# Kernel optimization log

Measured on AMD Instinct MI355X. Metric: run time of the kernel, lower is better.

The kernel has to match this reference:

```python
import jax, jax.numpy as jnp
import numpy as np

R, N, F, L = 4, 4096, 64, 2  # relations, entities, feature dim, conv layers


def setup_inputs() -> dict:
    key = jax.random.key(0)
    k_adj, k_feat, k_w, k_rel = jax.random.split(key, 4)
    adjacency = jax.random.uniform(k_adj, (R, N, N), dtype=jnp.float32)
    features = jax.random.normal(k_feat, (N, F), dtype=jnp.float32)
    # per-layer conv weights, torch.rand init: [L, R, F_out, F_in]
    conv_weights = jax.random.uniform(k_w, (L, R, F, F), dtype=jnp.float32)
    # DistMult relation matrices initialized as diag(rand(F)) per torch code
    diag_vals = jax.random.uniform(k_rel, (R, F), dtype=jnp.float32)
    rel_matrices = jax.vmap(jnp.diag)(diag_vals)  # [R, F, F]
    return {
        "adjacency": adjacency,
        "features": features,
        "conv_weights": conv_weights,
        "rel_matrices": rel_matrices,
    }


def reference(adjacency, features, conv_weights, rel_matrices):
    x = features  # [N, F]
    for l in range(conv_weights.shape[0]):
        # sum_r A[r] @ x @ W[l,r].T  -> [N, F]
        agg = jnp.einsum("rnm,mf->rnf", adjacency, x)
        y = jnp.einsum("rnf,rgf->ng", agg, conv_weights[l])
        x = jax.nn.sigmoid(y)
    # DistMult: res[r] = x @ M_r @ x.T  -> [R, N, N]
    xm = jnp.einsum("nf,rfg->rng", x, rel_matrices)
    return jnp.einsum("rng,mg->rnm", xm, x)
```

## Files before the change

### kernel.cpp

```cpp
#include <hip/hip_runtime.h>
#include <hip/hip_bf16.h>

#define NN 4096
#define FF 64
#define RR 4
#define KS 4

typedef __attribute__((ext_vector_type(8))) short bf16x8;
typedef __attribute__((ext_vector_type(4))) float f32x4;

__device__ __forceinline__ short f2bf(float f) {
  unsigned u = __builtin_bit_cast(unsigned, f);
  u = (u + 0x7fffu + ((u >> 16) & 1u)) >> 16;
  return (short)u;
}
__device__ __forceinline__ float bf2f(short s) {
  unsigned u = ((unsigned)(unsigned short)s) << 16;
  return __builtin_bit_cast(float, u);
}

__global__ void rgcn_prep(const float* __restrict__ feat, short* __restrict__ xfrag) {
  int kb = blockIdx.x;
  int t = threadIdx.x >> 6;
  int lane = threadIdx.x & 63;
  int lg = lane >> 4, li = lane & 15;
  bf16x8 pack;
#pragma unroll
  for (int e = 0; e < 8; e++) {
    int row = kb * 32 + lg * 8 + e;
    int col = t * 16 + li;
    pack[e] = f2bf(feat[row * FF + col]);
  }
  *(bf16x8*)(xfrag + (((size_t)(kb * 4 + t) * 64) + lane) * 8) = pack;
}

__global__ __launch_bounds__(256) void rgcn_agg(const float* __restrict__ A,
                                                const short* __restrict__ xfrag,
                                                float* __restrict__ aggp) {
  int w = threadIdx.x >> 6, lane = threadIdx.x & 63;
  int lg = lane >> 4, li = lane & 15;
  int r = blockIdx.y, ks = blockIdx.z;
  int n0 = blockIdx.x * 64 + w * 16;
  const float* Arow = A + ((size_t)r * NN + (n0 + li)) * NN;

  f32x4 acc0 = 0.f, acc1 = 0.f, acc2 = 0.f, acc3 = 0.f;

#pragma unroll 2
  for (int kk = 0; kk < 1024 / 32; kk++) {
    int k0 = ks * 1024 + kk * 32;
    const float4* pa = (const float4*)(Arow + k0 + lg * 8);
    float4 v0 = pa[0], v1 = pa[1];
    bf16x8 a;
    a[0] = f2bf(v0.x); a[1] = f2bf(v0.y); a[2] = f2bf(v0.z); a[3] = f2bf(v0.w);
    a[4] = f2bf(v1.x); a[5] = f2bf(v1.y); a[6] = f2bf(v1.z); a[7] = f2bf(v1.w);
    int kb = k0 >> 5;
    const short* xb = xfrag + (size_t)kb * 4 * 64 * 8 + lane * 8;
    bf16x8 b0 = *(const bf16x8*)(xb + 0 * 64 * 8);
    bf16x8 b1 = *(const bf16x8*)(xb + 1 * 64 * 8);
    bf16x8 b2 = *(const bf16x8*)(xb + 2 * 64 * 8);
    bf16x8 b3 = *(const bf16x8*)(xb + 3 * 64 * 8);
    acc0 = __builtin_amdgcn_mfma_f32_16x16x32_bf16(a, b0, acc0, 0, 0, 0);
    acc1 = __builtin_amdgcn_mfma_f32_16x16x32_bf16(a, b1, acc1, 0, 0, 0);
    acc2 = __builtin_amdgcn_mfma_f32_16x16x32_bf16(a, b2, acc2, 0, 0, 0);
    acc3 = __builtin_amdgcn_mfma_f32_16x16x32_bf16(a, b3, acc3, 0, 0, 0);
  }

  int pidx = ks * RR + r;
  float* out = aggp + ((size_t)pidx * NN + n0) * FF;
  f32x4 accs[4] = {acc0, acc1, acc2, acc3};
#pragma unroll
  for (int t = 0; t < 4; t++)
#pragma unroll
    for (int i = 0; i < 4; i++)
      out[(4 * lg + i) * FF + t * 16 + li] = accs[t][i];
}

__global__ __launch_bounds__(256) void rgcn_combine(const float* __restrict__ aggp,
                                                    const float* __restrict__ W,
                                                    short* __restrict__ xbf,
                                                    short* __restrict__ xfrag) {
  __shared__ float Wt[RR * FF * FF];
  int tid = threadIdx.x;
  for (int idx = tid; idx < RR * FF * FF; idx += 256) {
    int r = idx >> 12, g = (idx >> 6) & 63, f = idx & 63;
    Wt[(r * FF + f) * FF + g] = W[idx];
  }
  __syncthreads();

  int nl = tid >> 6, g = tid & 63;
  int n = blockIdx.x * 4 + nl;
  float acc = 0.f;
  for (int ksr = 0; ksr < KS * RR; ksr++) {
    int r = ksr & 3;
    float av = aggp[((size_t)ksr * NN + n) * FF + g];
#pragma unroll
    for (int f = 0; f < FF; f++)
      acc += __shfl(av, f) * Wt[(r * FF + f) * FF + g];
  }
  float xv = 1.f / (1.f + __expf(-acc));
  xbf[n * FF + g] = f2bf(xv);
  int kb = n >> 5, kr = n & 31, lg2 = kr >> 3, e = kr & 7, t = g >> 4, li = g & 15;
  xfrag[(((size_t)(kb * 4 + t) * 64) + lg2 * 16 + li) * 8 + e] = f2bf(xv);
}

__global__ __launch_bounds__(256) void rgcn_xm(const short* __restrict__ xbf,
                                               const float* __restrict__ M,
                                               short* __restrict__ xm) {
  __shared__ float Ml[FF * FF];
  int tid = threadIdx.x;
  int r = blockIdx.y;
  for (int idx = tid; idx < FF * FF; idx += 256) Ml[idx] = M[r * FF * FF + idx];
  __syncthreads();
  int nl = tid >> 6, g = tid & 63;
  int n = blockIdx.x * 4 + nl;
  float xv = bf2f(xbf[n * FF + g]);
  float acc = 0.f;
#pragma unroll
  for (int f = 0; f < FF; f++) acc += __shfl(xv, f) * Ml[f * FF + g];
  xm[((size_t)r * NN + n) * FF + g] = f2bf(acc);
}

__global__ __launch_bounds__(256) void rgcn_distmult(const short* __restrict__ xm,
                                                     const short* __restrict__ xbf,
                                                     float* __restrict__ out) {
  int w = threadIdx.x >> 6, lane = threadIdx.x & 63;
  int lg = lane >> 4, li = lane & 15;
  int r = blockIdx.z;
  int n0 = blockIdx.y * 64 + w * 16;
  int m0 = blockIdx.x * 64;

  const short* pa = xm + ((size_t)r * NN + n0 + li) * FF + lg * 8;
  bf16x8 a0 = *(const bf16x8*)(pa);
  bf16x8 a1 = *(const bf16x8*)(pa + 32);

  f32x4 acc0 = 0.f, acc1 = 0.f, acc2 = 0.f, acc3 = 0.f;
#pragma unroll
  for (int s = 0; s < 2; s++) {
    bf16x8 af = (s == 0) ? a0 : a1;
    const short* pb = xbf + (size_t)(m0 + li) * FF + s * 32 + lg * 8;
    bf16x8 b0 = *(const bf16x8*)(pb + 0 * 16 * FF);
    bf16x8 b1 = *(const bf16x8*)(pb + 1 * 16 * FF);
    bf16x8 b2 = *(const bf16x8*)(pb + 2 * 16 * FF);
    bf16x8 b3 = *(const bf16x8*)(pb + 3 * 16 * FF);
    acc0 = __builtin_amdgcn_mfma_f32_16x16x32_bf16(af, b0, acc0, 0, 0, 0);
    acc1 = __builtin_amdgcn_mfma_f32_16x16x32_bf16(af, b1, acc1, 0, 0, 0);
    acc2 = __builtin_amdgcn_mfma_f32_16x16x32_bf16(af, b2, acc2, 0, 0, 0);
    acc3 = __builtin_amdgcn_mfma_f32_16x16x32_bf16(af, b3, acc3, 0, 0, 0);
  }
  f32x4 accs[4] = {acc0, acc1, acc2, acc3};
#pragma unroll
  for (int t = 0; t < 4; t++)
#pragma unroll
    for (int i = 0; i < 4; i++)
      out[((size_t)r * NN + (n0 + 4 * lg + i)) * NN + m0 + t * 16 + li] = accs[t][i];
}

extern "C" void kernel_launch(void* const* d_in, const int* in_sizes, int n_in,
                              void* d_out, int out_size, void* d_ws, size_t ws_size,
                              hipStream_t stream) {
  const float* A = (const float*)d_in[0];
  const float* feat = (const float*)d_in[1];
  const float* Wc = (const float*)d_in[2];
  const float* M = (const float*)d_in[3];
  float* out = (float*)d_out;

  char* ws = (char*)d_ws;
  short* xfrag = (short*)ws;
  short* xbf   = (short*)(ws + (512 << 10));
  short* xmb   = (short*)(ws + (1 << 20));
  float* aggp = (float*)d_out;

  rgcn_prep<<<dim3(128), 256, 0, stream>>>(feat, xfrag);
  for (int l = 0; l < 2; l++) {
    rgcn_agg<<<dim3(64, RR, KS), 256, 0, stream>>>(A, xfrag, aggp);
    rgcn_combine<<<dim3(NN / 4), 256, 0, stream>>>(aggp, Wc + (size_t)l * RR * FF * FF, xbf, xfrag);
  }
  rgcn_xm<<<dim3(NN / 4, RR), 256, 0, stream>>>(xbf, M, xmb);
  rgcn_distmult<<<dim3(64, 64, RR), 256, 0, stream>>>(xmb, xbf, out);
}
```

Baseline: 784.3 us.

## Reassociate RGCN layer as A@(xW^T) with atomic accumulation across relations

```diff
diff --git a/kernel.cpp b/kernel.cpp
--- a/kernel.cpp
+++ b/kernel.cpp
@@ -19,29 +19,39 @@
   return __builtin_bit_cast(float, u);
 }
 
-__global__ void rgcn_prep(const float* __restrict__ feat, short* __restrict__ xfrag) {
-  int kb = blockIdx.x;
-  int t = threadIdx.x >> 6;
-  int lane = threadIdx.x & 63;
-  int lg = lane >> 4, li = lane & 15;
-  bf16x8 pack;
+__global__ __launch_bounds__(256) void rgcn_z(const float* __restrict__ x,
+                                              const float* __restrict__ W,
+                                              short* __restrict__ zfrag,
+                                              float* __restrict__ y) {
+  int tid = threadIdx.x;
+  int r = blockIdx.y;
+  int gtid = (blockIdx.y * (NN / 4) + blockIdx.x) * 256 + tid;
+  if (gtid < NN * FF) y[gtid] = 0.f;
+
+  int nl = tid >> 6, g = tid & 63;
+  int n = blockIdx.x * 4 + nl;
+  const float* xr = x + n * FF;
+  const float* wr = W + (r * FF + g) * FF;
+  float acc = 0.f;
 #pragma unroll
-  for (int e = 0; e < 8; e++) {
-    int row = kb * 32 + lg * 8 + e;
-    int col = t * 16 + li;
-    pack[e] = f2bf(feat[row * FF + col]);
+  for (int f = 0; f < FF; f += 4) {
+    float4 xv = *(const float4*)(xr + f);
+    float4 wv = *(const float4*)(wr + f);
+    acc += xv.x * wv.x + xv.y * wv.y + xv.z * wv.z + xv.w * wv.w;
   }
-  *(bf16x8*)(xfrag + (((size_t)(kb * 4 + t) * 64) + lane) * 8) = pack;
+  int kb = n >> 5, r5 = n & 31, lg = r5 >> 3, e = r5 & 7, t = g >> 4, li = g & 15;
+  zfrag[(size_t)r * NN * FF + (((kb * 4 + t) * 64) + lg * 16 + li) * 8 + e] = f2bf(acc);
 }
 
 __global__ __launch_bounds__(256) void rgcn_agg(const float* __restrict__ A,
-                                                const short* __restrict__ xfrag,
-                                                float* __restrict__ aggp) {
+                                                const short* __restrict__ zfrag,
+                                                float* __restrict__ y) {
   int w = threadIdx.x >> 6, lane = threadIdx.x & 63;
   int lg = lane >> 4, li = lane & 15;
   int r = blockIdx.y, ks = blockIdx.z;
   int n0 = blockIdx.x * 64 + w * 16;
   const float* Arow = A + ((size_t)r * NN + (n0 + li)) * NN;
+  const short* zf = zfrag + (size_t)r * NN * FF;
 
   f32x4 acc0 = 0.f, acc1 = 0.f, acc2 = 0.f, acc3 = 0.f;
 
@@ -54,7 +64,7 @@
     a[0] = f2bf(v0.x); a[1] = f2bf(v0.y); a[2] = f2bf(v0.z); a[3] = f2bf(v0.w);
     a[4] = f2bf(v1.x); a[5] = f2bf(v1.y); a[6] = f2bf(v1.z); a[7] = f2bf(v1.w);
     int kb = k0 >> 5;
-    const short* xb = xfrag + (size_t)kb * 4 * 64 * 8 + lane * 8;
+    const short* xb = zf + (size_t)kb * 4 * 64 * 8 + lane * 8;
     bf16x8 b0 = *(const bf16x8*)(xb + 0 * 64 * 8);
     bf16x8 b1 = *(const bf16x8*)(xb + 1 * 64 * 8);
     bf16x8 b2 = *(const bf16x8*)(xb + 2 * 64 * 8);
@@ -65,58 +75,38 @@
     acc3 = __builtin_amdgcn_mfma_f32_16x16x32_bf16(a, b3, acc3, 0, 0, 0);
   }
 
-  int pidx = ks * RR + r;
-  float* out = aggp + ((size_t)pidx * NN + n0) * FF;
+  float* yo = y + (size_t)n0 * FF;
   f32x4 accs[4] = {acc0, acc1, acc2, acc3};
 #pragma unroll
   for (int t = 0; t < 4; t++)
 #pragma unroll
     for (int i = 0; i < 4; i++)
-      out[(4 * lg + i) * FF + t * 16 + li] = accs[t][i];
+      atomicAdd(&yo[(4 * lg + i) * FF + t * 16 + li], accs[t][i]);
 }
 
-__global__ __launch_bounds__(256) void rgcn_combine(const float* __restrict__ aggp,
-                                                    const float* __restrict__ W,
-                                                    short* __restrict__ xbf,
-                                                    short* __restrict__ xfrag) {
-  __shared__ float Wt[RR * FF * FF];
-  int tid = threadIdx.x;
-  for (int idx = tid; idx < RR * FF * FF; idx += 256) {
-    int r = idx >> 12, g = (idx >> 6) & 63, f = idx & 63;
-    Wt[(r * FF + f) * FF + g] = W[idx];
-  }
-  __syncthreads();
-
-  int nl = tid >> 6, g = tid & 63;
-  int n = blockIdx.x * 4 + nl;
-  float acc = 0.f;
-  for (int ksr = 0; ksr < KS * RR; ksr++) {
-    int r = ksr & 3;
-    float av = aggp[((size_t)ksr * NN + n) * FF + g];
-#pragma unroll
-    for (int f = 0; f < FF; f++)
-      acc += __shfl(av, f) * Wt[(r * FF + f) * FF + g];
-  }
-  float xv = 1.f / (1.f + __expf(-acc));
-  xbf[n * FF + g] = f2bf(xv);
-  int kb = n >> 5, kr = n & 31, lg2 = kr >> 3, e = kr & 7, t = g >> 4, li = g & 15;
-  xfrag[(((size_t)(kb * 4 + t) * 64) + lg2 * 16 + li) * 8 + e] = f2bf(xv);
+__global__ __launch_bounds__(256) void rgcn_sig(const float* __restrict__ y,
+                                                float* __restrict__ xf,
+                                                short* __restrict__ xbf) {
+  int i = blockIdx.x * 256 + threadIdx.x;
+  float v = 1.f / (1.f + __expf(-y[i]));
+  xf[i] = v;
+  xbf[i] = f2bf(v);
 }
 
 __global__ __launch_bounds__(256) void rgcn_xm(const short* __restrict__ xbf,
                                                const float* __restrict__ M,
                                                short* __restrict__ xm) {
-  __shared__ float Ml[FF * FF];
-  int tid = threadIdx.x;
   int r = blockIdx.y;
-  for (int idx = tid; idx < FF * FF; idx += 256) Ml[idx] = M[r * FF * FF + idx];
-  __syncthreads();
-  int nl = tid >> 6, g = tid & 63;
+  int nl = threadIdx.x >> 6, g = threadIdx.x & 63;
   int n = blockIdx.x * 4 + nl;
-  float xv = bf2f(xbf[n * FF + g]);
+  const bf16x8* xr = (const bf16x8*)(xbf + n * FF);
+  bf16x8 xv0 = xr[0], xv1 = xr[1], xv2 = xr[2], xv3 = xr[3];
+  bf16x8 xv4 = xr[4], xv5 = xr[5], xv6 = xr[6], xv7 = xr[7];
+  bf16x8 xv[8] = {xv0, xv1, xv2, xv3, xv4, xv5, xv6, xv7};
+  const float* Mr = M + r * FF * FF;
   float acc = 0.f;
 #pragma unroll
-  for (int f = 0; f < FF; f++) acc += __shfl(xv, f) * Ml[f * FF + g];
+  for (int f = 0; f < FF; f++) acc += bf2f(xv[f >> 3][f & 7]) * Mr[f * FF + g];
   xm[((size_t)r * NN + n) * FF + g] = f2bf(acc);
 }
 
@@ -165,15 +155,18 @@
   float* out = (float*)d_out;
 
   char* ws = (char*)d_ws;
-  short* xfrag = (short*)ws;
-  short* xbf   = (short*)(ws + (512 << 10));
-  short* xmb   = (short*)(ws + (1 << 20));
-  float* aggp = (float*)d_out;
+  short* zfrag = (short*)ws;
+  float* y     = (float*)(ws + (2u << 20));
+  float* xf    = (float*)(ws + (3u << 20));
+  short* xbf   = (short*)(ws + (4u << 20));
+  short* xmb   = (short*)(ws + (5u << 20));
 
-  rgcn_prep<<<dim3(128), 256, 0, stream>>>(feat, xfrag);
+  const float* xin = feat;
   for (int l = 0; l < 2; l++) {
-    rgcn_agg<<<dim3(64, RR, KS), 256, 0, stream>>>(A, xfrag, aggp);
-    rgcn_combine<<<dim3(NN / 4), 256, 0, stream>>>(aggp, Wc + (size_t)l * RR * FF * FF, xbf, xfrag);
+    rgcn_z<<<dim3(NN / 4, RR), 256, 0, stream>>>(xin, Wc + (size_t)l * RR * FF * FF, zfrag, y);
+    rgcn_agg<<<dim3(64, RR, KS), 256, 0, stream>>>(A, zfrag, y);
+    rgcn_sig<<<dim3(NN * FF / 256), 256, 0, stream>>>(y, xf, xbf);
+    xin = xf;
   }
   rgcn_xm<<<dim3(NN / 4, RR), 256, 0, stream>>>(xbf, M, xmb);
   rgcn_distmult<<<dim3(64, 64, RR), 256, 0, stream>>>(xmb, xbf, out);
```

New measurement: 673.9 us. 1.16x faster.
